# Performance work log

Measured on AMD Instinct MI355X. Metric: run time of the kernel, lower is better.

Reference implementation:

```python
import jax, jax.numpy as jnp
import numpy as np

B, L, S, H, E = 2, 2048, 2048, 8, 64
MASK_SCALE = 10000.0
TAU_MIN, TAU_MAX = 0.1, 5.0
THR_MIN, THR_MAX = 0.01, 0.99


def setup_inputs() -> dict:
    key = jax.random.key(0)
    ks = jax.random.split(key, 7)
    query = jax.random.normal(ks[0], (B, L, H, E), jnp.float32)
    k_ = jax.random.normal(ks[1], (B, S, H, E), jnp.float32)
    value = jax.random.normal(ks[2], (B, S, H, E), jnp.float32)
    mask_miss_k = jnp.zeros((B, S), jnp.float32)  # unused in forward
    mask_miss_q = jnp.zeros((B, L), jnp.float32)  # unused in forward
    pos = jnp.arange(B * L, dtype=jnp.int32).reshape(B, L, 1)  # monotone positions per batch
    hard_mask = jax.random.randint(ks[3], (L, S), 0, 2, dtype=jnp.int32)
    hard_mask = hard_mask.at[jnp.arange(L), jnp.arange(S)].set(1)  # keep diagonal open
    # learned parameters / stochastic state
    phi = jax.random.normal(ks[4], (H, L, S), jnp.float32)  # DAG edge logits (per head)
    log_tau_gs = jnp.asarray(np.log(2.0), jnp.float32)
    threshold = jnp.asarray(0.5, jnp.float32)
    u = jax.random.uniform(ks[5], (H, L, S), jnp.float32, 1e-6, 1.0 - 1e-6)  # Gumbel base noise
    return {"query": query, "key": k_, "value": value, "mask_miss_k": mask_miss_k,
            "mask_miss_q": mask_miss_q, "pos": pos, "causal_mask": 1,
            "hard_mask": hard_mask, "phi": phi, "log_tau_gs": log_tau_gs,
            "threshold": threshold, "u": u}


def reference(query, key, value, mask_miss_k, mask_miss_q, pos, causal_mask,
              hard_mask, phi, log_tau_gs, threshold, u):
    e = query.shape[-1]
    scale = 1.0 / np.sqrt(e)
    # scores: (B, H, L, S)
    scores = jnp.einsum('blhe,bshe->bhls', query, key)
    if causal_mask:
        p = pos[..., 0]  # (B, L)
        causal = jnp.where(p[:, None, :] > p[:, :, None], -jnp.inf, 0.0).astype(scores.dtype)
        scores = scores + causal[:, None, :, :]
    # Gumbel-sigmoid relaxed DAG mask
    tau = jnp.clip(jnp.exp(log_tau_gs), TAU_MIN, TAU_MAX)
    gumbel = jnp.log(u + 1e-8) - jnp.log(1.0 - u + 1e-8)
    m_relaxed = jax.nn.sigmoid((gumbel + phi) / tau)  # (H, L, S)
    thr = jnp.clip(threshold, THR_MIN, THR_MAX)
    dag_add = MASK_SCALE * jnp.minimum(m_relaxed - thr, 0.0)  # <=0 additive penalty
    scores = scores + dag_add[None, :, :, :]
    # hard mask applied pre-softmax as -inf
    scores = jnp.where(hard_mask[None, None, :, :] == 0, -jnp.inf, scores)
    att = jax.nn.softmax(scale * scores, axis=-1)  # dropout p=0 (eval)
    out = jnp.einsum('bhls,bshe->blhe', att, value)  # (B, L, H, E)
    return out
```

## Files before the change

kernel.cpp:

```cpp
#include <hip/hip_runtime.h>


#define Bz 2
#define Lz 2048
#define Sz 2048
#define Hz 8
#define Ez 64
#define NSEG 4
#define NEG_BIG (-1e30f)

typedef __attribute__((ext_vector_type(8))) short short8;
typedef __attribute__((ext_vector_type(4))) short short4v;
typedef __attribute__((ext_vector_type(4))) float f32x4;

__device__ __forceinline__ float fast_rcp(float x) { return __builtin_amdgcn_rcpf(x); }

__device__ __forceinline__ short f2bf(float x) {
    unsigned bits = __builtin_bit_cast(unsigned, x);
    bits += 0x7FFFu + ((bits >> 16) & 1u);
    return (short)(bits >> 16);
}

__device__ __forceinline__ void gl_lds16(const void* g, void* l) {
    __builtin_amdgcn_global_load_lds(
        (const __attribute__((address_space(1))) void*)g,
        (__attribute__((address_space(3))) void*)l,
        16, 0, 0);
}

__global__ void pack_qk(const float* __restrict__ q, const float* __restrict__ k,
                        short* __restrict__ qp, short* __restrict__ kp,
                        const int* __restrict__ hm, const int* __restrict__ caus_p,
                        unsigned long long* __restrict__ dmask)
{
    const int t = blockIdx.x * 256 + threadIdx.x;
    const float4 qv = ((const float4*)q)[t];
    const float4 kv = ((const float4*)k)[t];
    const int e4   = t & 15;
    const int rest = t >> 4;
    const int h    = rest & 7;
    const int bl   = rest >> 3;
    const int b    = bl >> 11;
    const int l    = bl & 2047;
    const int o    = ((b*Hz + h)*Lz + l)*Ez + e4*4;
    short4v qo, ko;
    qo[0] = f2bf(qv.x*0.125f); qo[1] = f2bf(qv.y*0.125f);
    qo[2] = f2bf(qv.z*0.125f); qo[3] = f2bf(qv.w*0.125f);
    ko[0] = f2bf(kv.x); ko[1] = f2bf(kv.y); ko[2] = f2bf(kv.z); ko[3] = f2bf(kv.w);
    *(short4v*)&qp[o] = qo;
    *(short4v*)&kp[o] = ko;

    {
        const int lane = threadIdx.x & 63;
        const int lrow = blockIdx.x;
        const int w0   = (threadIdx.x >> 6) * 8;
        const int causal = *caus_p;
#pragma unroll
        for (int i = 0; i < 8; ++i) {
            const int tt = w0 + i;
            int dead;
            if (causal && (tt*64 > lrow)) {
                dead = 1;
            } else {
                const int s = tt*64 + lane;
                dead = (hm[lrow*Sz + s] == 0) || (causal && (s > lrow));
            }
            const unsigned long long m = __ballot(dead);
            if (lane == 0) dmask[lrow*32 + tt] = m;
        }
    }
}

__global__ void pack_vt(const float* __restrict__ v, short* __restrict__ vt)
{
    const int blk = blockIdx.x;
    const int st  = blk & 63;
    const int h   = (blk >> 6) & 7;
    const int b   = blk >> 9;
    const int s0  = st * 32;
    const int e   = threadIdx.x & 63;
    const int sc  = threadIdx.x >> 6;
    short8 ov;
#pragma unroll
    for (int j = 0; j < 8; ++j) {
        const int s = s0 + sc*8 + j;
        ov[j] = f2bf(v[((b*Sz + s)*Hz + h)*Ez + e]);
    }
    *(short8*)&vt[((b*Hz + h)*Ez + e)*Sz + s0 + sc*8] = ov;
}

__global__ __launch_bounds__(256, 2) void attn_main(
    const float* __restrict__ phi, const float* __restrict__ u,
    const unsigned long long* __restrict__ dmask, const int* __restrict__ causal_p,
    const float* __restrict__ log_tau_p, const float* __restrict__ thr_p,
    const short* __restrict__ qp, const short* __restrict__ kp,
    const short* __restrict__ vt,
    float* __restrict__ Op, float* __restrict__ Mp, float* __restrict__ Lp)
{
    const int lane  = threadIdx.x & 63;
    const int wslot = threadIdx.x >> 6;
    const int seg   = wslot;
    const int qq    = blockIdx.x;
    const int h     = qq & 7;
    const int c     = 127 - (qq >> 3);
    const int l_base = c * 16;
    const int ln    = lane & 15;
    const int quad  = lane >> 4;

    const int causal = *causal_p;
    float tau = __expf(*log_tau_p);
    tau = fminf(fmaxf(tau, 0.1f), 5.0f);
    const float inv_tau = 1.0f / tau;
    const float thr = fminf(fmaxf(*thr_p, 0.01f), 0.99f);

    short8 qf[2][2];
#pragma unroll
    for (int b = 0; b < 2; ++b)
#pragma unroll
        for (int k = 0; k < 2; ++k)
            qf[b][k] = *(const short8*)&qp[((b*Hz + h)*Lz + l_base + ln)*Ez + k*32 + quad*8];

    f32x4 O[2][4];
    float m_r[2][4], l_r[2][4];
#pragma unroll
    for (int b = 0; b < 2; ++b) {
#pragma unroll
        for (int ne = 0; ne < 4; ++ne) { f32x4 z = {0.f,0.f,0.f,0.f}; O[b][ne] = z; }
#pragma unroll
        for (int r = 0; r < 4; ++r) { m_r[b][r] = -INFINITY; l_r[b][r] = 0.f; }
    }

    const int T = causal ? (((l_base + 15) >> 6) + 1) : (Sz >> 6);

    __shared__ __align__(16) short plds[4][16*72];
    __shared__ __align__(16) float stage[4][2048];
    short* myp = &plds[wslot][0];
    float* st  = &stage[wslot][0];

    const size_t rowbase = (size_t)(h*Lz + l_base)*Sz;
    const int    lrow    = (lane >> 4);
    const int    lcol    = (ln << 2);

#define ISSUE_TILE(tt)                                                          \
    {                                                                           \
        const size_t gofs = rowbase + (size_t)((tt) << 6) + lcol;               \
        _Pragma("unroll")                                                       \
        for (int j = 0; j < 4; ++j) {                                           \
            const size_t r8 = (size_t)(j*4 + lrow) * Sz;                        \
            gl_lds16(&phi[gofs + r8], st + j*256);                              \
            gl_lds16(&u[gofs + r8],   st + 1024 + j*256);                       \
        }                                                                       \
    }

    if (seg < T) ISSUE_TILE(seg);

    for (int t = seg; t < T; t += NSEG) {
        const int s0 = t << 6;

        unsigned long long dmc[4];
#pragma unroll
        for (int r = 0; r < 4; ++r)
            dmc[r] = dmask[(l_base + quad*4 + r)*(Sz/64) + t];

        asm volatile("s_waitcnt vmcnt(0)" ::: "memory");
        __builtin_amdgcn_sched_barrier(0);

        float dg[4][4];
#pragma unroll
        for (int nt = 0; nt < 4; ++nt)
#pragma unroll
            for (int r = 0; r < 4; ++r) {
                const int idx = (quad*4 + r)*64 + nt*16 + ln;
                const float ph = st[idx];
                const float uv = st[1024 + idx];
                const float g  = __logf((uv + 1e-8f) * fast_rcp(1.0f - uv + 1e-8f));
                const float z  = (g + ph) * inv_tau;
                const float sg = fast_rcp(1.0f + __expf(-z));
                const float d  = 1250.0f * fminf(sg - thr, 0.0f);
                const bool dead = (dmc[r] >> (nt*16 + ln)) & 1ull;
                dg[nt][r] = dead ? -INFINITY : d;
            }

        asm volatile("s_waitcnt lgkmcnt(0)" ::: "memory");
        __builtin_amdgcn_sched_barrier(0);
        if (t + NSEG < T) ISSUE_TILE(t + NSEG);

#pragma unroll
        for (int b = 0; b < 2; ++b) {
            short8 kf[4][2];
#pragma unroll
            for (int nt = 0; nt < 4; ++nt)
#pragma unroll
                for (int k = 0; k < 2; ++k)
                    kf[nt][k] = *(const short8*)&kp[((b*Hz + h)*Sz + s0 + nt*16 + ln)*Ez + k*32 + quad*8];

            f32x4 Sc[4];
#pragma unroll
            for (int nt = 0; nt < 4; ++nt) {
                f32x4 z4 = {0.f,0.f,0.f,0.f};
                z4 = __builtin_amdgcn_mfma_f32_16x16x32_bf16(qf[b][0], kf[nt][0], z4, 0, 0, 0);
                Sc[nt] = __builtin_amdgcn_mfma_f32_16x16x32_bf16(qf[b][1], kf[nt][1], z4, 0, 0, 0);
            }

            float mx[4];
#pragma unroll
            for (int r = 0; r < 4; ++r) mx[r] = -INFINITY;
#pragma unroll
            for (int nt = 0; nt < 4; ++nt)
#pragma unroll
                for (int r = 0; r < 4; ++r) {
                    Sc[nt][r] += dg[nt][r];
                    mx[r] = fmaxf(mx[r], Sc[nt][r]);
                }
#pragma unroll
            for (int r = 0; r < 4; ++r)
#pragma unroll
                for (int o = 1; o < 16; o <<= 1)
                    mx[r] = fmaxf(mx[r], __shfl_xor(mx[r], o, 16));

            float al[4], mn[4];
#pragma unroll
            for (int r = 0; r < 4; ++r) {
                mn[r] = fmaxf(m_r[b][r], mx[r]);
                al[r] = __expf(fmaxf(m_r[b][r], NEG_BIG) - fmaxf(mn[r], NEG_BIG));
                m_r[b][r] = mn[r];
            }

            float ps[4] = {0.f, 0.f, 0.f, 0.f};
#pragma unroll
            for (int nt = 0; nt < 4; ++nt)
#pragma unroll
                for (int r = 0; r < 4; ++r) {
                    const float p = __expf(Sc[nt][r] - fmaxf(mn[r], NEG_BIG));
                    ps[r] += p;
                    myp[(quad*4 + r)*72 + nt*16 + ln] = f2bf(p);
                }
#pragma unroll
            for (int r = 0; r < 4; ++r) {
#pragma unroll
                for (int o = 1; o < 16; o <<= 1)
                    ps[r] += __shfl_xor(ps[r], o, 16);
                l_r[b][r] = l_r[b][r] * al[r] + ps[r];
            }
#pragma unroll
            for (int ne = 0; ne < 4; ++ne)
#pragma unroll
                for (int r = 0; r < 4; ++r)
                    O[b][ne][r] *= al[r];

            short8 pa[2];
#pragma unroll
            for (int k = 0; k < 2; ++k)
                pa[k] = *(const short8*)&myp[ln*72 + k*32 + quad*8];

#pragma unroll
            for (int ne = 0; ne < 4; ++ne) {
                const short8 v0 = *(const short8*)&vt[((b*Hz + h)*Ez + ne*16 + ln)*Sz + s0 + quad*8];
                const short8 v1 = *(const short8*)&vt[((b*Hz + h)*Ez + ne*16 + ln)*Sz + s0 + 32 + quad*8];
                O[b][ne] = __builtin_amdgcn_mfma_f32_16x16x32_bf16(pa[0], v0, O[b][ne], 0, 0, 0);
                O[b][ne] = __builtin_amdgcn_mfma_f32_16x16x32_bf16(pa[1], v1, O[b][ne], 0, 0, 0);
            }
        }
    }

#pragma unroll
    for (int b = 0; b < 2; ++b) {
#pragma unroll
        for (int ne = 0; ne < 4; ++ne)
#pragma unroll
            for (int r = 0; r < 4; ++r) {
                const int l = l_base + quad*4 + r;
                Op[(((seg*2 + b)*Hz + h)*Lz + l)*Ez + ne*16 + ln] = O[b][ne][r];
            }
        if (ln == 0) {
#pragma unroll
            for (int r = 0; r < 4; ++r) {
                const int l = l_base + quad*4 + r;
                Mp[((seg*2 + b)*Hz + h)*Lz + l] = m_r[b][r];
                Lp[((seg*2 + b)*Hz + h)*Lz + l] = l_r[b][r];
            }
        }
    }
}

__global__ void merge_k(const float* __restrict__ Op, const float* __restrict__ Mp,
                        const float* __restrict__ Lp, float* __restrict__ out)
{
    const int t = blockIdx.x * 256 + threadIdx.x;
    const int e4   = (t & 15) * 4;
    const int rest = t >> 4;
    const int h    = rest & 7;
    const int bl   = rest >> 3;
    const int b    = bl >> 11;
    const int l    = bl & 2047;

    float ms[NSEG], ls[NSEG], m = -INFINITY;
#pragma unroll
    for (int s = 0; s < NSEG; ++s) {
        const int idx = ((s*2 + b)*Hz + h)*Lz + l;
        ms[s] = Mp[idx];
        ls[s] = Lp[idx];
        m = fmaxf(m, ms[s]);
    }
    const float mg = fmaxf(m, NEG_BIG);
    float den = 0.f, a0 = 0.f, a1 = 0.f, a2 = 0.f, a3 = 0.f;
#pragma unroll
    for (int s = 0; s < NSEG; ++s) {
        const float w = __expf(fmaxf(ms[s], NEG_BIG) - mg);
        den += w * ls[s];
        const float4 ov = *(const float4*)&Op[(((s*2 + b)*Hz + h)*Lz + l)*Ez + e4];
        a0 += w * ov.x; a1 += w * ov.y; a2 += w * ov.z; a3 += w * ov.w;
    }
    const float rd = 1.0f / den;
    float4 res;
    res.x = a0 * rd; res.y = a1 * rd; res.z = a2 * rd; res.w = a3 * rd;
    *(float4*)&out[((b*Lz + l)*Hz + h)*Ez + e4] = res;
}

extern "C" void kernel_launch(void* const* d_in, const int* in_sizes, int n_in,
                              void* d_out, int out_size, void* d_ws, size_t ws_size,
                              hipStream_t stream)
{
    const float* q     = (const float*)d_in[0];
    const float* k     = (const float*)d_in[1];
    const float* v     = (const float*)d_in[2];
    const int*   caus  = (const int*)d_in[6];
    const int*   hm    = (const int*)d_in[7];
    const float* phi   = (const float*)d_in[8];
    const float* ltau  = (const float*)d_in[9];
    const float* thr   = (const float*)d_in[10];
    const float* u     = (const float*)d_in[11];

    char* ws = (char*)d_ws;
    short* qp = (short*)(ws);
    short* kp = (short*)(ws + (size_t)( 4u << 20));
    short* vt = (short*)(ws + (size_t)( 8u << 20));
    float* Op = (float*)(ws + (size_t)(12u << 20));
    float* Mp = (float*)(ws + (size_t)(44u << 20));
    float* Lp = (float*)(ws + (size_t)(44u << 20) + (512u << 10));
    unsigned long long* dmask = (unsigned long long*)(ws + (size_t)(45u << 20));

    pack_qk <<<2048, 256, 0, stream>>>(q, k, qp, kp, hm, caus, dmask);
    pack_vt <<<1024, 256, 0, stream>>>(v, vt);
    attn_main<<<1024, 256, 0, stream>>>(phi, u, dmask, caus, ltau, thr, qp, kp, vt, Op, Mp, Lp);
    merge_k <<<2048, 256, 0, stream>>>(Op, Mp, Lp, (float*)d_out);
}
```

Measured before the change: 361.0 us.

## Split DAG-mask generation into a separate fp16 kernel ahead of attention

```diff
diff --git a/kernel.cpp b/kernel.cpp
--- a/kernel.cpp
+++ b/kernel.cpp
@@ -1,4 +1,5 @@
 #include <hip/hip_runtime.h>
+#include <hip/hip_fp16.h>
 
 
 #define Bz 2
@@ -21,11 +22,9 @@
     return (short)(bits >> 16);
 }
 
-__device__ __forceinline__ void gl_lds16(const void* g, void* l) {
-    __builtin_amdgcn_global_load_lds(
-        (const __attribute__((address_space(1))) void*)g,
-        (__attribute__((address_space(3))) void*)l,
-        16, 0, 0);
+__device__ __forceinline__ int tri_prefix(int lt) {
+    const int m = lt >> 2;
+    return lt + 2*m*(m-1) + (lt & 3)*m;
 }
 
 __global__ void pack_qk(const float* __restrict__ q, const float* __restrict__ k,
@@ -89,36 +88,103 @@
     *(short8*)&vt[((b*Hz + h)*Ez + e)*Sz + s0 + sc*8] = ov;
 }
 
-__global__ __launch_bounds__(256, 2) void attn_main(
+__global__ __launch_bounds__(256) void dg_gen(
     const float* __restrict__ phi, const float* __restrict__ u,
-    const unsigned long long* __restrict__ dmask, const int* __restrict__ causal_p,
+    const unsigned long long* __restrict__ dmask, const int* __restrict__ caus_p,
     const float* __restrict__ log_tau_p, const float* __restrict__ thr_p,
-    const short* __restrict__ qp, const short* __restrict__ kp,
-    const short* __restrict__ vt,
-    float* __restrict__ Op, float* __restrict__ Mp, float* __restrict__ Lp)
+    unsigned short* __restrict__ dgp)
 {
     const int lane  = threadIdx.x & 63;
     const int wslot = threadIdx.x >> 6;
-    const int seg   = wslot;
-    const int qq    = blockIdx.x;
-    const int h     = qq & 7;
-    const int c     = 127 - (qq >> 3);
-    const int l_base = c * 16;
+    const int h     = blockIdx.x & 7;
+    const int lt    = 127 - (blockIdx.x >> 3);
+    const int quad  = lane >> 4;
     const int ln    = lane & 15;
-    const int quad  = lane >> 4;
-
-    const int causal = *causal_p;
+
+    const int causal = *caus_p;
     float tau = __expf(*log_tau_p);
     tau = fminf(fmaxf(tau, 0.1f), 5.0f);
     const float inv_tau = 1.0f / tau;
     const float thr = fminf(fmaxf(*thr_p, 0.01f), 0.99f);
 
-    short8 qf[2][2];
-#pragma unroll
-    for (int b = 0; b < 2; ++b)
-#pragma unroll
-        for (int k = 0; k < 2; ++k)
-            qf[b][k] = *(const short8*)&qp[((b*Hz + h)*Lz + l_base + ln)*Ez + k*32 + quad*8];
+    const int C  = lt >> 2;
+    const int Tg = causal ? (C + 1) : (Sz >> 6);
+    const int tb = causal ? (h*2112 + tri_prefix(lt)) : (h*128 + lt)*32;
+
+    __shared__ float myd_all[4][16*68];
+    float* myd = myd_all[wslot];
+
+    for (int t = wslot; t < Tg; t += 4) {
+        unsigned long long dmc[4];
+        f32x4 pv[4], uv[4];
+#pragma unroll
+        for (int i = 0; i < 4; ++i) {
+            const int l = lt*16 + quad*4 + i;
+            const size_t off = ((size_t)(h*Lz + l))*Sz + (size_t)(t*64 + ln*4);
+            pv[i]  = *(const f32x4*)&phi[off];
+            uv[i]  = *(const f32x4*)&u[off];
+            dmc[i] = dmask[l*32 + t];
+        }
+#pragma unroll
+        for (int i = 0; i < 4; ++i) {
+            f32x4 dv;
+#pragma unroll
+            for (int cc = 0; cc < 4; ++cc) {
+                const float uvv = uv[i][cc];
+                const float g   = __logf((uvv + 1e-8f) * fast_rcp(1.0f - uvv + 1e-8f));
+                const float z   = (g + pv[i][cc]) * inv_tau;
+                const float sg  = fast_rcp(1.0f + __expf(-z));
+                const float d   = 1250.0f * fminf(sg - thr, 0.0f);
+                const bool dead = (dmc[i] >> (ln*4 + cc)) & 1ull;
+                dv[cc] = dead ? -INFINITY : d;
+            }
+            *(f32x4*)&myd[(quad*4 + i)*68 + ln*4] = dv;
+        }
+        asm volatile("s_waitcnt lgkmcnt(0)" ::: "memory");
+        __builtin_amdgcn_sched_barrier(0);
+
+        unsigned out[8];
+#pragma unroll
+        for (int r = 0; r < 4; ++r) {
+            const float v0 = myd[(quad*4 + r)*68 +  0 + ln];
+            const float v1 = myd[(quad*4 + r)*68 + 16 + ln];
+            const float v2 = myd[(quad*4 + r)*68 + 32 + ln];
+            const float v3 = myd[(quad*4 + r)*68 + 48 + ln];
+            out[r*2]   = (unsigned)__half_as_ushort(__float2half(v0))
+                       | ((unsigned)__half_as_ushort(__float2half(v1)) << 16);
+            out[r*2+1] = (unsigned)__half_as_ushort(__float2half(v2))
+                       | ((unsigned)__half_as_ushort(__float2half(v3)) << 16);
+        }
+        const size_t o16 = ((size_t)(tb + t) << 10) + (size_t)lane*16;
+        uint4 w0, w1;
+        w0.x = out[0]; w0.y = out[1]; w0.z = out[2]; w0.w = out[3];
+        w1.x = out[4]; w1.y = out[5]; w1.z = out[6]; w1.w = out[7];
+        *(uint4*)&dgp[o16]     = w0;
+        *(uint4*)&dgp[o16 + 8] = w1;
+    }
+}
+
+__global__ __launch_bounds__(256, 3) void attn_main(
+    const unsigned short* __restrict__ dgp, const int* __restrict__ causal_p,
+    const short* __restrict__ qp, const short* __restrict__ kp,
+    const short* __restrict__ vt,
+    float* __restrict__ Op, float* __restrict__ Mp, float* __restrict__ Lp)
+{
+    const int lane  = threadIdx.x & 63;
+    const int wslot = threadIdx.x >> 6;
+    const int qq    = blockIdx.x;
+    const int seg   = qq & 3;
+    const int cc    = qq >> 2;
+    const int h     = cc & 7;
+    const int C     = 31 - (cc >> 3);
+    const int l_base = C*64 + wslot*16;
+    const int ln    = lane & 15;
+    const int quad  = lane >> 4;
+
+    const int causal = *causal_p;
+    const int lt = C*4 + wslot;
+    const int tb = causal ? (h*2112 + tri_prefix(lt)) : (h*128 + lt)*32;
+    const int T  = causal ? (C + 1) : (Sz >> 6);
 
     f32x4 O[2][4];
     float m_r[2][4], l_r[2][4];
@@ -130,76 +196,55 @@
         for (int r = 0; r < 4; ++r) { m_r[b][r] = -INFINITY; l_r[b][r] = 0.f; }
     }
 
-    const int T = causal ? (((l_base + 15) >> 6) + 1) : (Sz >> 6);
-
     __shared__ __align__(16) short plds[4][16*72];
-    __shared__ __align__(16) float stage[4][2048];
     short* myp = &plds[wslot][0];
-    float* st  = &stage[wslot][0];
-
-    const size_t rowbase = (size_t)(h*Lz + l_base)*Sz;
-    const int    lrow    = (lane >> 4);
-    const int    lcol    = (ln << 2);
-
-#define ISSUE_TILE(tt)                                                          \
-    {                                                                           \
-        const size_t gofs = rowbase + (size_t)((tt) << 6) + lcol;               \
-        _Pragma("unroll")                                                       \
-        for (int j = 0; j < 4; ++j) {                                           \
-            const size_t r8 = (size_t)(j*4 + lrow) * Sz;                        \
-            gl_lds16(&phi[gofs + r8], st + j*256);                              \
-            gl_lds16(&u[gofs + r8],   st + 1024 + j*256);                       \
-        }                                                                       \
-    }
-
-    if (seg < T) ISSUE_TILE(seg);
 
     for (int t = seg; t < T; t += NSEG) {
         const int s0 = t << 6;
 
-        unsigned long long dmc[4];
-#pragma unroll
-        for (int r = 0; r < 4; ++r)
-            dmc[r] = dmask[(l_base + quad*4 + r)*(Sz/64) + t];
-
-        asm volatile("s_waitcnt vmcnt(0)" ::: "memory");
-        __builtin_amdgcn_sched_barrier(0);
-
-        float dg[4][4];
-#pragma unroll
-        for (int nt = 0; nt < 4; ++nt)
-#pragma unroll
-            for (int r = 0; r < 4; ++r) {
-                const int idx = (quad*4 + r)*64 + nt*16 + ln;
-                const float ph = st[idx];
-                const float uv = st[1024 + idx];
-                const float g  = __logf((uv + 1e-8f) * fast_rcp(1.0f - uv + 1e-8f));
-                const float z  = (g + ph) * inv_tau;
-                const float sg = fast_rcp(1.0f + __expf(-z));
-                const float d  = 1250.0f * fminf(sg - thr, 0.0f);
-                const bool dead = (dmc[r] >> (nt*16 + ln)) & 1ull;
-                dg[nt][r] = dead ? -INFINITY : d;
-            }
-
-        asm volatile("s_waitcnt lgkmcnt(0)" ::: "memory");
-        __builtin_amdgcn_sched_barrier(0);
-        if (t + NSEG < T) ISSUE_TILE(t + NSEG);
+        const size_t doff = ((size_t)(tb + t) << 10) + (size_t)lane*16;
+        const uint4 dA = *(const uint4*)&dgp[doff];
+        const uint4 dB = *(const uint4*)&dgp[doff + 8];
+
+        float dgf[4][4];
 
 #pragma unroll
         for (int b = 0; b < 2; ++b) {
+            short8 qfb[2];
+#pragma unroll
+            for (int k = 0; k < 2; ++k)
+                qfb[k] = *(const short8*)&qp[((b*Hz + h)*Lz + l_base + ln)*Ez + k*32 + quad*8];
             short8 kf[4][2];
 #pragma unroll
             for (int nt = 0; nt < 4; ++nt)
 #pragma unroll
                 for (int k = 0; k < 2; ++k)
                     kf[nt][k] = *(const short8*)&kp[((b*Hz + h)*Sz + s0 + nt*16 + ln)*Ez + k*32 + quad*8];
+            short8 vv[4][2];
+#pragma unroll
+            for (int ne = 0; ne < 4; ++ne) {
+                vv[ne][0] = *(const short8*)&vt[((b*Hz + h)*Ez + ne*16 + ln)*Sz + s0 + quad*8];
+                vv[ne][1] = *(const short8*)&vt[((b*Hz + h)*Ez + ne*16 + ln)*Sz + s0 + 32 + quad*8];
+            }
+
+            if (b == 0) {
+#pragma unroll
+                for (int r = 0; r < 4; ++r) {
+                    const unsigned dw0 = (r < 2) ? (&dA.x)[r*2]     : (&dB.x)[(r-2)*2];
+                    const unsigned dw1 = (r < 2) ? (&dA.x)[r*2 + 1] : (&dB.x)[(r-2)*2 + 1];
+                    dgf[0][r] = __half2float(__ushort_as_half((unsigned short)(dw0 & 0xffffu)));
+                    dgf[1][r] = __half2float(__ushort_as_half((unsigned short)(dw0 >> 16)));
+                    dgf[2][r] = __half2float(__ushort_as_half((unsigned short)(dw1 & 0xffffu)));
+                    dgf[3][r] = __half2float(__ushort_as_half((unsigned short)(dw1 >> 16)));
+                }
+            }
 
             f32x4 Sc[4];
 #pragma unroll
             for (int nt = 0; nt < 4; ++nt) {
                 f32x4 z4 = {0.f,0.f,0.f,0.f};
-                z4 = __builtin_amdgcn_mfma_f32_16x16x32_bf16(qf[b][0], kf[nt][0], z4, 0, 0, 0);
-                Sc[nt] = __builtin_amdgcn_mfma_f32_16x16x32_bf16(qf[b][1], kf[nt][1], z4, 0, 0, 0);
+                z4 = __builtin_amdgcn_mfma_f32_16x16x32_bf16(qfb[0], kf[nt][0], z4, 0, 0, 0);
+                Sc[nt] = __builtin_amdgcn_mfma_f32_16x16x32_bf16(qfb[1], kf[nt][1], z4, 0, 0, 0);
             }
 
             float mx[4];
@@ -209,7 +254,7 @@
             for (int nt = 0; nt < 4; ++nt)
 #pragma unroll
                 for (int r = 0; r < 4; ++r) {
-                    Sc[nt][r] += dg[nt][r];
+                    Sc[nt][r] += dgf[nt][r];
                     mx[r] = fmaxf(mx[r], Sc[nt][r]);
                 }
 #pragma unroll
@@ -255,10 +300,8 @@
 
 #pragma unroll
             for (int ne = 0; ne < 4; ++ne) {
-                const short8 v0 = *(const short8*)&vt[((b*Hz + h)*Ez + ne*16 + ln)*Sz + s0 + quad*8];
-                const short8 v1 = *(const short8*)&vt[((b*Hz + h)*Ez + ne*16 + ln)*Sz + s0 + 32 + quad*8];
-                O[b][ne] = __builtin_amdgcn_mfma_f32_16x16x32_bf16(pa[0], v0, O[b][ne], 0, 0, 0);
-                O[b][ne] = __builtin_amdgcn_mfma_f32_16x16x32_bf16(pa[1], v1, O[b][ne], 0, 0, 0);
+                O[b][ne] = __builtin_amdgcn_mfma_f32_16x16x32_bf16(pa[0], vv[ne][0], O[b][ne], 0, 0, 0);
+                O[b][ne] = __builtin_amdgcn_mfma_f32_16x16x32_bf16(pa[1], vv[ne][1], O[b][ne], 0, 0, 0);
             }
         }
     }
@@ -339,9 +382,11 @@
     float* Mp = (float*)(ws + (size_t)(44u << 20));
     float* Lp = (float*)(ws + (size_t)(44u << 20) + (512u << 10));
     unsigned long long* dmask = (unsigned long long*)(ws + (size_t)(45u << 20));
+    unsigned short* dgp = (unsigned short*)(ws + (size_t)(46u << 20));
 
     pack_qk <<<2048, 256, 0, stream>>>(q, k, qp, kp, hm, caus, dmask);
     pack_vt <<<1024, 256, 0, stream>>>(v, vt);
-    attn_main<<<1024, 256, 0, stream>>>(phi, u, dmask, caus, ltau, thr, qp, kp, vt, Op, Mp, Lp);
+    dg_gen  <<<1024, 256, 0, stream>>>(phi, u, dmask, caus, ltau, thr, dgp);
+    attn_main<<<1024, 256, 0, stream>>>(dgp, caus, qp, kp, vt, Op, Mp, Lp);
     merge_k <<<2048, 256, 0, stream>>>(Op, Mp, Lp, (float*)d_out);
 }
```

Result: slower. 396.8 us (+9.9%).
